# Performance work log

Hardware: AMD Instinct MI355X
Metric: run time of the kernel (lower is better)

Reference implementation:

```python
import jax, jax.numpy as jnp
import numpy as np

B, S, D, H = 4, 2048, 1024, 16
HD = D // H


def setup_inputs() -> dict:
    key = jax.random.key(0)
    ks = jax.random.split(key, 9)
    s = 1.0 / np.sqrt(D)
    return {
        "x": jax.random.normal(ks[0], (B, S, D), dtype=jnp.float32),
        "Wq": jax.random.normal(ks[1], (D, D), dtype=jnp.float32) * s,
        "bq": jnp.zeros((D,), dtype=jnp.float32),
        "Wk": jax.random.normal(ks[2], (D, D), dtype=jnp.float32) * s,
        "bk": jnp.zeros((D,), dtype=jnp.float32),
        "Wv": jax.random.normal(ks[3], (D, D), dtype=jnp.float32) * s,
        "bv": jnp.zeros((D,), dtype=jnp.float32),
        "Wo": jax.random.normal(ks[4], (D, D), dtype=jnp.float32) * s,
        "bo": jnp.zeros((D,), dtype=jnp.float32),
    }


def reference(x, Wq, bq, Wk, bk, Wv, bv, Wo, bo):
    b, s, d = x.shape
    # project and split heads -> [b, h, s, hd]
    def split_heads(t):
        return t.reshape(b, s, H, HD).transpose(0, 2, 1, 3)
    q = split_heads(x @ Wq.T + bq)
    k = split_heads(x @ Wk.T + bk)
    v = split_heads(x @ Wv.T + bv)
    scale = 1.0 / np.sqrt(HD).astype(np.float32)
    att = jnp.einsum('bhqd,bhkd->bhqk', q, k) * scale
    causal = jnp.tril(jnp.ones((s, s), dtype=bool))
    att = jnp.where(causal[None, None], att, -jnp.inf)
    att = jax.nn.softmax(att, axis=-1)
    out = jnp.einsum('bhqk,bhkd->bhqd', att, v)  # [b,h,s,hd]
    out = out.transpose(0, 2, 1, 3).reshape(b, s, d)
    return out @ Wo.T + bo
```

## Files before the change

kernel.cpp:

```cpp
#include <hip/hip_runtime.h>
#include <hip/hip_bf16.h>
#include <math.h>

typedef __hip_bfloat16 bf16;
typedef __attribute__((ext_vector_type(8))) __bf16 bf16x8;
typedef __attribute__((ext_vector_type(4))) float f32x4;

__device__ __forceinline__ void gload_lds16(const void* g, void* l) {
  __builtin_amdgcn_global_load_lds(
      (const __attribute__((address_space(1))) unsigned int*)g,
      (__attribute__((address_space(3))) unsigned int*)l, 16, 0, 0);
}

__global__ void cvt_bf16(const float* __restrict__ in, bf16* __restrict__ out, int n) {
  int idx = (blockIdx.x * blockDim.x + threadIdx.x) * 8;
  if (idx >= n) return;
  float4 v0 = *(const float4*)(in + idx);
  float4 v1 = *(const float4*)(in + idx + 4);
  alignas(16) bf16 tmp[8];
  tmp[0] = __float2bfloat16(v0.x); tmp[1] = __float2bfloat16(v0.y);
  tmp[2] = __float2bfloat16(v0.z); tmp[3] = __float2bfloat16(v0.w);
  tmp[4] = __float2bfloat16(v1.x); tmp[5] = __float2bfloat16(v1.y);
  tmp[6] = __float2bfloat16(v1.z); tmp[7] = __float2bfloat16(v1.w);
  *(uint4*)(out + idx) = *(const uint4*)tmp;
}

__global__ void prep_w(const float* __restrict__ Wq, const float* __restrict__ Wk,
                       const float* __restrict__ Wv, const float* __restrict__ Wo,
                       const float* __restrict__ bq, const float* __restrict__ bk,
                       const float* __restrict__ bv,
                       bf16* __restrict__ wqkv, bf16* __restrict__ wo16,
                       float* __restrict__ b3) {
  const float QSCL = 0.125f * 1.4426950408889634f;
  const int bi = blockIdx.x;
  if (bi < 2048) {
    const int seg = bi >> 9;
    const int idx = ((bi & 511) * 256 + threadIdx.x) * 8;
    const float* src = seg == 0 ? Wq : seg == 1 ? Wk : seg == 2 ? Wv : Wo;
    bf16* dst = seg < 3 ? wqkv + (size_t)seg * 1048576 : wo16;
    const float m = (seg == 0) ? QSCL : 1.0f;
    float4 v0 = *(const float4*)(src + idx);
    float4 v1 = *(const float4*)(src + idx + 4);
    alignas(16) bf16 tmp[8];
    tmp[0] = __float2bfloat16(v0.x * m); tmp[1] = __float2bfloat16(v0.y * m);
    tmp[2] = __float2bfloat16(v0.z * m); tmp[3] = __float2bfloat16(v0.w * m);
    tmp[4] = __float2bfloat16(v1.x * m); tmp[5] = __float2bfloat16(v1.y * m);
    tmp[6] = __float2bfloat16(v1.z * m); tmp[7] = __float2bfloat16(v1.w * m);
    *(uint4*)(dst + idx) = *(const uint4*)tmp;
  } else {
    const int i = (bi - 2048) * 256 + threadIdx.x;
    if (i < 3072)
      b3[i] = i < 1024 ? bq[i] * QSCL : i < 2048 ? bk[i - 1024] : bv[i - 2048];
  }
}

template<int MODE>
__global__ __launch_bounds__(512, 2) void gemm3(
    const bf16* __restrict__ A, const bf16* __restrict__ Bw,
    const float* __restrict__ bias, void* __restrict__ Cout,
    bf16* __restrict__ vt, int N, int K)
{
  constexpr int SLOT = 24576;
  __shared__ bf16 lds[3 * SLOT];
  const int tid = threadIdx.x;
  const int wave = tid >> 6, lane = tid & 63;
  const int lhi = lane >> 4, llo = lane & 15;
  const int wr = wave >> 2, wc = wave & 3;

  const int xcd = blockIdx.x & 7;
  const int l = blockIdx.x >> 3;
  const int row0 = (xcd * 8 + (l & 7)) * 128;
  const int col0 = (l >> 3) * 256;

  auto stageA = [&](int t) {
    bf16* s = &lds[(t % 3) * SLOT];
    const size_t k0 = (size_t)t << 6;
#pragma unroll
    for (int j = 0; j < 2; ++j) {
      int i = j * 512 + tid;
      int r = i >> 3, gl = (i & 7) ^ (r & 7);
      gload_lds16(A + (size_t)(row0 + r) * K + k0 + gl * 8, s + i * 8);
    }
  };
  auto stageBh = [&](int t, int half) {
    bf16* s = &lds[(t % 3) * SLOT] + 8192;
    const size_t k0 = (size_t)t << 6;
#pragma unroll
    for (int j = 0; j < 2; ++j) {
      int i = half * 1024 + j * 512 + tid;
      int r = i >> 3, gl = (i & 7) ^ (r & 7);
      gload_lds16(Bw + (size_t)(col0 + r) * K + k0 + gl * 8, s + i * 8);
    }
  };

  f32x4 acc[4][4] = {};
  const int T = K >> 6;

  stageA(0); stageBh(0, 0); stageBh(0, 1);
  stageA(1); stageBh(1, 0); stageBh(1, 1);
  asm volatile("s_waitcnt vmcnt(6)" ::: "memory");
  __builtin_amdgcn_s_barrier();

  for (int t = 0; t < T; ++t) {
    const bf16* sa = &lds[(t % 3) * SLOT];
    const bf16* sb = sa + 8192;

    bf16x8 af[4][2], bfr[2][2];
#pragma unroll
    for (int m = 0; m < 4; ++m)
#pragma unroll
      for (int kk = 0; kk < 2; ++kk) {
        int r = wr * 64 + m * 16 + llo;
        af[m][kk] = *(const bf16x8*)&sa[r * 64 + (((kk * 4 + lhi) ^ (r & 7)) << 3)];
      }
#pragma unroll
    for (int n = 0; n < 2; ++n)
#pragma unroll
      for (int kk = 0; kk < 2; ++kk) {
        int c = wc * 64 + n * 16 + llo;
        bfr[n][kk] = *(const bf16x8*)&sb[c * 64 + (((kk * 4 + lhi) ^ (c & 7)) << 3)];
      }
    if (t + 2 < T) { stageA(t + 2); stageBh(t + 2, 0); }
    __builtin_amdgcn_s_barrier();
    __builtin_amdgcn_s_setprio(1);
#pragma unroll
    for (int m = 0; m < 4; ++m)
#pragma unroll
      for (int n = 0; n < 2; ++n)
#pragma unroll
        for (int kk = 0; kk < 2; ++kk)
          acc[m][n] = __builtin_amdgcn_mfma_f32_16x16x32_bf16(af[m][kk], bfr[n][kk], acc[m][n], 0, 0, 0);
    __builtin_amdgcn_s_setprio(0);
    __builtin_amdgcn_s_barrier();

#pragma unroll
    for (int n = 0; n < 2; ++n)
#pragma unroll
      for (int kk = 0; kk < 2; ++kk) {
        int c = wc * 64 + 32 + n * 16 + llo;
        bfr[n][kk] = *(const bf16x8*)&sb[c * 64 + (((kk * 4 + lhi) ^ (c & 7)) << 3)];
      }
    if (t + 2 < T) stageBh(t + 2, 1);
    __builtin_amdgcn_s_barrier();
    __builtin_amdgcn_s_setprio(1);
#pragma unroll
    for (int m = 0; m < 4; ++m)
#pragma unroll
      for (int n = 0; n < 2; ++n)
#pragma unroll
        for (int kk = 0; kk < 2; ++kk)
          acc[m][2 + n] = __builtin_amdgcn_mfma_f32_16x16x32_bf16(af[m][kk], bfr[n][kk], acc[m][2 + n], 0, 0, 0);
    __builtin_amdgcn_s_setprio(0);
    if (t + 2 < T)      asm volatile("s_waitcnt vmcnt(6)" ::: "memory");
    else if (t + 1 < T) asm volatile("s_waitcnt vmcnt(0)" ::: "memory");
    __builtin_amdgcn_s_barrier();
  }

#pragma unroll
  for (int m = 0; m < 4; ++m)
#pragma unroll
    for (int n = 0; n < 4; ++n) {
      const int col = col0 + wc * 64 + (n & 1) * 16 + (n >> 1) * 32 + llo;
      const float bv = bias[col];
      const int rowbase = row0 + wr * 64 + m * 16 + lhi * 4;
      if (MODE == 1) {
#pragma unroll
        for (int j = 0; j < 4; ++j)
          ((float*)Cout)[(size_t)(rowbase + j) * N + col] = acc[m][n][j] + bv;
      } else if (col < 2048) {
#pragma unroll
        for (int j = 0; j < 4; ++j)
          ((bf16*)Cout)[(size_t)(rowbase + j) * N + col] = __float2bfloat16(acc[m][n][j] + bv);
      } else {
        const int hh = (col - 2048) >> 6, d = (col - 2048) & 63;
        const int bb = rowbase >> 11, s0 = rowbase & 2047;
        alignas(8) bf16 tmp[4];
#pragma unroll
        for (int j = 0; j < 4; ++j) tmp[j] = __float2bfloat16(acc[m][n][j] + bv);
        *(uint2*)&vt[((size_t)(bb * 16 + hh) * 64 + d) * 2048 + s0] = *(const uint2*)tmp;
      }
    }
}

__global__ __launch_bounds__(512, 4) void attn(
    const bf16* __restrict__ QKV, const bf16* __restrict__ Vt,
    bf16* __restrict__ O)
{
  const int S = 2048, DM = 3072;
  const int bx = blockIdx.x;
  const int qt = (bx < 256) ? (bx >> 6) : (7 - ((bx - 256) >> 6));
  const int rem = bx & 63, h = rem >> 2, b = rem & 3;
  const int tid = threadIdx.x, wave = tid >> 6, lane = tid & 63;
  const int lhi = lane >> 4, llo = lane & 15;

  __shared__ bf16 lK[2][64 * 64];
  __shared__ bf16 lV[2][64 * 64];
  __shared__ bf16 lP[8][32 * 64];

  const size_t rowb = (size_t)b * S;
  const int q0 = qt * 256;
  const int nkt = 4 * qt + 4;
  const int qw = q0 + wave * 32;
  const int dmax = (qw + 31) >> 6;

  bf16x8 vones;
#pragma unroll
  for (int i = 0; i < 8; ++i) vones[i] = (__bf16)1.0f;

  auto stageKV = [&](int buf, int kt) {
    const int i = tid;
    const int r = i >> 3;
    const int ce = ((i & 7) * 8) ^ ((r & 7) << 3);
    gload_lds16(&QKV[(rowb + (size_t)kt * 64 + r) * DM + 1024 + h * 64 + ce],
                &lK[buf][i * 8]);
    gload_lds16(&Vt[((size_t)(b * 16 + h) * 64 + r) * S + kt * 64 + ce],
                &lV[buf][i * 8]);
  };

  bf16x8 qf[2][2];
#pragma unroll
  for (int hh = 0; hh < 2; ++hh)
#pragma unroll
    for (int kk = 0; kk < 2; ++kk)
      qf[hh][kk] = *(const bf16x8*)&QKV[(rowb + qw + hh * 16 + llo) * DM
                                        + h * 64 + kk * 32 + lhi * 8];

  f32x4 o_acc[2][4] = {};
  f32x4 o_l[2] = {};

  stageKV(0, 0);
  for (int kt = 0; kt < nkt; ++kt) {
    __syncthreads();
    if (kt + 1 < nkt) stageKV((kt + 1) & 1, kt + 1);
    if (kt > dmax) continue;
    const int buf = kt & 1;

    f32x4 s[2][4] = {};
#pragma unroll
    for (int kk = 0; kk < 2; ++kk)
#pragma unroll
      for (int n = 0; n < 4; ++n) {
        const int kr = n * 16 + llo;
        bf16x8 kf = *(const bf16x8*)&lK[buf][kr * 64 + ((kk * 32 + lhi * 8) ^ ((kr & 7) << 3))];
        s[0][n] = __builtin_amdgcn_mfma_f32_16x16x32_bf16(kf, qf[0][kk], s[0][n], 0, 0, 0);
        s[1][n] = __builtin_amdgcn_mfma_f32_16x16x32_bf16(kf, qf[1][kk], s[1][n], 0, 0, 0);
      }

#pragma unroll
    for (int hh = 0; hh < 2; ++hh) {
      if (kt >= ((qw + hh * 16) >> 6)) {
        const int lim = qw + hh * 16 + llo - kt * 64;
#pragma unroll
        for (int n = 0; n < 4; ++n)
#pragma unroll
          for (int j = 0; j < 4; ++j)
            if (n * 16 + lhi * 4 + j > lim) s[hh][n][j] = -INFINITY;
      }

#pragma unroll
      for (int n = 0; n < 4; ++n)
#pragma unroll
        for (int j = 0; j < 4; ++j)
          s[hh][n][j] = exp2f(s[hh][n][j]);

#pragma unroll
      for (int n = 0; n < 4; ++n) {
        alignas(8) bf16 tmp[4];
#pragma unroll
        for (int j = 0; j < 4; ++j) tmp[j] = __float2bfloat16(s[hh][n][j]);
        const int g = (n * 4 + lhi) ^ ((llo & 7) << 1);
        *(uint2*)&lP[wave][(hh * 16 + llo) * 64 + g * 4] = *(const uint2*)tmp;
      }
    }

#pragma unroll
    for (int kk = 0; kk < 2; ++kk) {
      const int g0 = (kk * 8 + lhi * 2) ^ ((llo & 7) << 1);
      bf16x8 pf0 = *(const bf16x8*)&lP[wave][(llo) * 64 + g0 * 4];
      bf16x8 pf1 = *(const bf16x8*)&lP[wave][(16 + llo) * 64 + g0 * 4];
#pragma unroll
      for (int n = 0; n < 4; ++n) {
        const int vr = n * 16 + llo;
        bf16x8 vf = *(const bf16x8*)&lV[buf][vr * 64 + ((kk * 32 + lhi * 8) ^ ((vr & 7) << 3))];
        o_acc[0][n] = __builtin_amdgcn_mfma_f32_16x16x32_bf16(vf, pf0, o_acc[0][n], 0, 0, 0);
        o_acc[1][n] = __builtin_amdgcn_mfma_f32_16x16x32_bf16(vf, pf1, o_acc[1][n], 0, 0, 0);
      }
      o_l[0] = __builtin_amdgcn_mfma_f32_16x16x32_bf16(vones, pf0, o_l[0], 0, 0, 0);
      o_l[1] = __builtin_amdgcn_mfma_f32_16x16x32_bf16(vones, pf1, o_l[1], 0, 0, 0);
    }
  }

#pragma unroll
  for (int hh = 0; hh < 2; ++hh) {
    const float inv = 1.0f / o_l[hh][0];
    const size_t orow = (rowb + qw + hh * 16 + llo) * 1024 + h * 64;
#pragma unroll
    for (int n = 0; n < 4; ++n) {
      alignas(8) bf16 tmp[4];
#pragma unroll
      for (int j = 0; j < 4; ++j) tmp[j] = __float2bfloat16(o_acc[hh][n][j] * inv);
      *(uint2*)&O[orow + n * 16 + lhi * 4] = *(const uint2*)tmp;
    }
  }
}

extern "C" void kernel_launch(void* const* d_in, const int* in_sizes, int n_in,
                              void* d_out, int out_size, void* d_ws, size_t ws_size,
                              hipStream_t stream) {
  const float* x  = (const float*)d_in[0];
  const float* Wq = (const float*)d_in[1];
  const float* bq = (const float*)d_in[2];
  const float* Wk = (const float*)d_in[3];
  const float* bk = (const float*)d_in[4];
  const float* Wv = (const float*)d_in[5];
  const float* bv = (const float*)d_in[6];
  const float* Wo = (const float*)d_in[7];
  const float* bo = (const float*)d_in[8];

  const int Bb = 4, S = 2048, D = 1024;
  const int M = Bb * S;
  const int N3 = 3 * D;

  bf16* x16  = (bf16*)d_ws;
  bf16* wqkv = x16 + (size_t)M * D;
  bf16* wo16 = wqkv + (size_t)3 * D * D;
  bf16* qkv  = wo16 + (size_t)D * D;
  bf16* vt   = qkv + (size_t)M * N3;
  float* b3  = (float*)(vt + (size_t)M * D);
  size_t needed = ((size_t)M * D * 3 + 4 * (size_t)D * D + (size_t)M * N3) * 2 + 3072 * 4;
  if (ws_size < needed) return;

  cvt_bf16<<<(M * D) / (8 * 256), 256, 0, stream>>>(x, x16, M * D);
  prep_w<<<2060, 256, 0, stream>>>(Wq, Wk, Wv, Wo, bq, bk, bv, wqkv, wo16, b3);

  gemm3<0><<<(M / 128) * (N3 / 256), 512, 0, stream>>>(x16, wqkv, b3, qkv, vt, N3, D);
  attn<<<dim3(512, 1, 1), 512, 0, stream>>>(qkv, vt, x16);
  gemm3<1><<<(M / 128) * (D / 256), 512, 0, stream>>>(x16, wo16, bo, d_out, nullptr, D, D);
}
```

Before: 175.0 us.

## Rewrite projection GEMM with 4 waves, K=32 stages and larger per-wave tiles

Replaces the 8-wave 128x256 GEMM with a 4-wave kernel in which each wave computes a full 128x64 slice (8x4 MFMA tiles). The K step per stage shrinks from 64 to 32, so each stage is loaded with a single staging call. The LDS layout changes from a row-major XOR-swizzled layout to a k-chunk-major layout, and the split-B half-stage barriers are removed. The goal is more MFMA work per fragment load and fewer barriers per iteration, at the cost of more accumulator registers per wave, possible LDS bank conflicts without the swizzle, and twice as many pipeline iterations.

```diff
diff --git a/kernel.cpp b/kernel.cpp
--- a/kernel.cpp
+++ b/kernel.cpp
@@ -55,114 +55,79 @@
 }
 
 template<int MODE>
-__global__ __launch_bounds__(512, 2) void gemm3(
+__global__ __launch_bounds__(256, 2) void gemm4(
     const bf16* __restrict__ A, const bf16* __restrict__ Bw,
     const float* __restrict__ bias, void* __restrict__ Cout,
     bf16* __restrict__ vt, int N, int K)
 {
-  constexpr int SLOT = 24576;
+  constexpr int SLOT = 12288;
   __shared__ bf16 lds[3 * SLOT];
   const int tid = threadIdx.x;
-  const int wave = tid >> 6, lane = tid & 63;
+  const int wc = tid >> 6, lane = tid & 63;
   const int lhi = lane >> 4, llo = lane & 15;
-  const int wr = wave >> 2, wc = wave & 3;
 
   const int xcd = blockIdx.x & 7;
   const int l = blockIdx.x >> 3;
   const int row0 = (xcd * 8 + (l & 7)) * 128;
   const int col0 = (l >> 3) * 256;
 
-  auto stageA = [&](int t) {
+  auto stage = [&](int t) {
     bf16* s = &lds[(t % 3) * SLOT];
-    const size_t k0 = (size_t)t << 6;
+    const size_t k0 = (size_t)t << 5;
 #pragma unroll
     for (int j = 0; j < 2; ++j) {
-      int i = j * 512 + tid;
-      int r = i >> 3, gl = (i & 7) ^ (r & 7);
-      gload_lds16(A + (size_t)(row0 + r) * K + k0 + gl * 8, s + i * 8);
+      int c = j * 256 + tid;
+      gload_lds16(A + (size_t)(row0 + (c & 127)) * K + k0 + (c >> 7) * 8, s + c * 8);
+    }
+#pragma unroll
+    for (int j = 0; j < 4; ++j) {
+      int c = j * 256 + tid;
+      gload_lds16(Bw + (size_t)(col0 + (c & 255)) * K + k0 + (c >> 8) * 8,
+                  s + 4096 + c * 8);
     }
   };
-  auto stageBh = [&](int t, int half) {
-    bf16* s = &lds[(t % 3) * SLOT] + 8192;
-    const size_t k0 = (size_t)t << 6;
-#pragma unroll
-    for (int j = 0; j < 2; ++j) {
-      int i = half * 1024 + j * 512 + tid;
-      int r = i >> 3, gl = (i & 7) ^ (r & 7);
-      gload_lds16(Bw + (size_t)(col0 + r) * K + k0 + gl * 8, s + i * 8);
-    }
-  };
-
-  f32x4 acc[4][4] = {};
-  const int T = K >> 6;
-
-  stageA(0); stageBh(0, 0); stageBh(0, 1);
-  stageA(1); stageBh(1, 0); stageBh(1, 1);
+
+  f32x4 acc[8][4] = {};
+  const int T = K >> 5;
+
+  stage(0); stage(1);
   asm volatile("s_waitcnt vmcnt(6)" ::: "memory");
   __builtin_amdgcn_s_barrier();
 
   for (int t = 0; t < T; ++t) {
     const bf16* sa = &lds[(t % 3) * SLOT];
-    const bf16* sb = sa + 8192;
-
-    bf16x8 af[4][2], bfr[2][2];
-#pragma unroll
-    for (int m = 0; m < 4; ++m)
-#pragma unroll
-      for (int kk = 0; kk < 2; ++kk) {
-        int r = wr * 64 + m * 16 + llo;
-        af[m][kk] = *(const bf16x8*)&sa[r * 64 + (((kk * 4 + lhi) ^ (r & 7)) << 3)];
-      }
-#pragma unroll
-    for (int n = 0; n < 2; ++n)
-#pragma unroll
-      for (int kk = 0; kk < 2; ++kk) {
-        int c = wc * 64 + n * 16 + llo;
-        bfr[n][kk] = *(const bf16x8*)&sb[c * 64 + (((kk * 4 + lhi) ^ (c & 7)) << 3)];
-      }
-    if (t + 2 < T) { stageA(t + 2); stageBh(t + 2, 0); }
-    __builtin_amdgcn_s_barrier();
+    const bf16* sb = sa + 4096;
+
+    bf16x8 af[8], bfr[4];
+#pragma unroll
+    for (int m = 0; m < 8; ++m)
+      af[m] = *(const bf16x8*)&sa[(lhi * 128 + m * 16 + llo) * 8];
+#pragma unroll
+    for (int n = 0; n < 4; ++n)
+      bfr[n] = *(const bf16x8*)&sb[(lhi * 256 + wc * 64 + n * 16 + llo) * 8];
+
+    if (t + 2 < T) stage(t + 2);
+
     __builtin_amdgcn_s_setprio(1);
 #pragma unroll
-    for (int m = 0; m < 4; ++m)
-#pragma unroll
-      for (int n = 0; n < 2; ++n)
-#pragma unroll
-        for (int kk = 0; kk < 2; ++kk)
-          acc[m][n] = __builtin_amdgcn_mfma_f32_16x16x32_bf16(af[m][kk], bfr[n][kk], acc[m][n], 0, 0, 0);
+    for (int m = 0; m < 8; ++m)
+#pragma unroll
+      for (int n = 0; n < 4; ++n)
+        acc[m][n] = __builtin_amdgcn_mfma_f32_16x16x32_bf16(af[m], bfr[n], acc[m][n], 0, 0, 0);
     __builtin_amdgcn_s_setprio(0);
-    __builtin_amdgcn_s_barrier();
-
-#pragma unroll
-    for (int n = 0; n < 2; ++n)
-#pragma unroll
-      for (int kk = 0; kk < 2; ++kk) {
-        int c = wc * 64 + 32 + n * 16 + llo;
-        bfr[n][kk] = *(const bf16x8*)&sb[c * 64 + (((kk * 4 + lhi) ^ (c & 7)) << 3)];
-      }
-    if (t + 2 < T) stageBh(t + 2, 1);
-    __builtin_amdgcn_s_barrier();
-    __builtin_amdgcn_s_setprio(1);
-#pragma unroll
-    for (int m = 0; m < 4; ++m)
-#pragma unroll
-      for (int n = 0; n < 2; ++n)
-#pragma unroll
-        for (int kk = 0; kk < 2; ++kk)
-          acc[m][2 + n] = __builtin_amdgcn_mfma_f32_16x16x32_bf16(af[m][kk], bfr[n][kk], acc[m][2 + n], 0, 0, 0);
-    __builtin_amdgcn_s_setprio(0);
+
     if (t + 2 < T)      asm volatile("s_waitcnt vmcnt(6)" ::: "memory");
     else if (t + 1 < T) asm volatile("s_waitcnt vmcnt(0)" ::: "memory");
     __builtin_amdgcn_s_barrier();
   }
 
 #pragma unroll
-  for (int m = 0; m < 4; ++m)
+  for (int m = 0; m < 8; ++m)
 #pragma unroll
     for (int n = 0; n < 4; ++n) {
-      const int col = col0 + wc * 64 + (n & 1) * 16 + (n >> 1) * 32 + llo;
+      const int col = col0 + wc * 64 + n * 16 + llo;
       const float bv = bias[col];
-      const int rowbase = row0 + wr * 64 + m * 16 + lhi * 4;
+      const int rowbase = row0 + m * 16 + lhi * 4;
       if (MODE == 1) {
 #pragma unroll
         for (int j = 0; j < 4; ++j)
@@ -333,7 +298,7 @@
   cvt_bf16<<<(M * D) / (8 * 256), 256, 0, stream>>>(x, x16, M * D);
   prep_w<<<2060, 256, 0, stream>>>(Wq, Wk, Wv, Wo, bq, bk, bv, wqkv, wo16, b3);
 
-  gemm3<0><<<(M / 128) * (N3 / 256), 512, 0, stream>>>(x16, wqkv, b3, qkv, vt, N3, D);
+  gemm4<0><<<(M / 128) * (N3 / 256), 256, 0, stream>>>(x16, wqkv, b3, qkv, vt, N3, D);
   attn<<<dim3(512, 1, 1), 512, 0, stream>>>(qkv, vt, x16);
-  gemm3<1><<<(M / 128) * (D / 256), 512, 0, stream>>>(x16, wo16, bo, d_out, nullptr, D, D);
-}
+  gemm4<1><<<(M / 128) * (D / 256), 256, 0, stream>>>(x16, wo16, bo, d_out, nullptr, D, D);
+}
```

Result: slower. 210.0 us (+20.0%).
